# Kernel optimization log

Hardware: AMD Instinct MI355X
Metric: run time of the kernel (lower is better)

The kernel has to match this reference:

```python
import jax, jax.numpy as jnp
import numpy as np


def setup_inputs() -> dict:
    key = jax.random.key(0)
    ks = jax.random.split(key, 8)
    N, E = 100000, 3200000
    IN, H, OUT = 256, 128, 64
    x = jax.random.normal(ks[0], (N, IN), dtype=jnp.float32)
    src = jax.random.randint(ks[1], (E,), 0, N, dtype=jnp.int64)
    dst = jax.random.randint(ks[2], (E,), 0, N, dtype=jnp.int64)
    # Glorot-ish scaled weights
    W1_self = jax.random.normal(ks[3], (IN, H), dtype=jnp.float32) / np.sqrt(IN)
    W1_neigh = jax.random.normal(ks[4], (IN, H), dtype=jnp.float32) / np.sqrt(IN)
    b1 = jnp.zeros((H,), dtype=jnp.float32)
    W2_self = jax.random.normal(ks[5], (H, OUT), dtype=jnp.float32) / np.sqrt(H)
    W2_neigh = jax.random.normal(ks[6], (H, OUT), dtype=jnp.float32) / np.sqrt(H)
    b2 = jnp.zeros((OUT,), dtype=jnp.float32)
    return {"x": x, "src": src, "dst": dst,
            "W1_self": W1_self, "W1_neigh": W1_neigh, "b1": b1,
            "W2_self": W2_self, "W2_neigh": W2_neigh, "b2": b2}


def _sage_mean(h, src, dst, W_self, W_neigh, b, deg_inv):
    # mean aggregation over in-neighbors (edges src -> dst)
    N = h.shape[0]
    agg = jax.ops.segment_sum(h[src], dst, num_segments=N)  # [N, F]
    h_neigh = agg * deg_inv[:, None]
    return h @ W_self + h_neigh @ W_neigh + b


def reference(x, src, dst, W1_self, W1_neigh, b1, W2_self, W2_neigh, b2):
    N = x.shape[0]
    deg = jax.ops.segment_sum(jnp.ones_like(dst, dtype=x.dtype), dst, num_segments=N)
    deg_inv = 1.0 / jnp.maximum(deg, 1.0)  # DGL clamps in-degree to >= 1
    h = _sage_mean(x, src, dst, W1_self, W1_neigh, b1, deg_inv)
    h = jax.nn.relu(h)
    h = _sage_mean(h, src, dst, W2_self, W2_neigh, b2, deg_inv)
    return h
```

## Files before the change

### kernel.cpp

```cpp
#include <hip/hip_runtime.h>
#include <hip/hip_bf16.h>


typedef unsigned int uint32;
typedef __attribute__((ext_vector_type(8))) short short8;
typedef __attribute__((ext_vector_type(4))) float f32x4;

#define NBMAX 1024
#define EPB   8192

#if defined(__has_builtin)
#if __has_builtin(__builtin_amdgcn_cvt_pk_f32_fp8) && __has_builtin(__builtin_amdgcn_cvt_pk_fp8_f32)
#define FP8_HW 1
#endif
#endif
#ifndef FP8_HW
#define FP8_HW 0
#endif

__device__ __forceinline__ unsigned short f2bf(float f) {
    unsigned u = __float_as_uint(f);
    u += 0x7fffu + ((u >> 16) & 1u);
    return (unsigned short)(u >> 16);
}
__device__ __forceinline__ uint32 pack2bf(float lo, float hi) {
    return (uint32)f2bf(lo) | ((uint32)f2bf(hi) << 16);
}
__device__ __forceinline__ float bf_lo(uint32 v) { return __uint_as_float(v << 16); }
__device__ __forceinline__ float bf_hi(uint32 v) { return __uint_as_float(v & 0xFFFF0000u); }

__device__ __forceinline__ unsigned char enc8(float v) {
#if FP8_HW
    return (unsigned char)(__builtin_amdgcn_cvt_pk_fp8_f32(v, v, 0, false) & 0xFF);
#else
    float g = v * 0x1p-120f;
    uint32 b = __float_as_uint(g);
    uint32 s = (b >> 24) & 0x80u;
    b &= 0x7fffffffu;
    b += 0x7ffffu + ((b >> 20) & 1u);
    int t = (int)(b >> 20) - 960;
    t = t < 0 ? 0 : (t > 126 ? 126 : t);
    return (unsigned char)(s | (uint32)t);
#endif
}
#if !FP8_HW
__device__ __forceinline__ float dec1(uint32 b) {
    uint32 bits = ((b & 0x80u) << 24) | ((b & 0x7fu) << 20);
    return __uint_as_float(bits) * 0x1p+120f;
}
#endif
__device__ __forceinline__ void dec_u32(uint32 u, float& f0, float& f1, float& f2, float& f3) {
#if FP8_HW
    auto lo = __builtin_amdgcn_cvt_pk_f32_fp8(u, false);
    auto hi = __builtin_amdgcn_cvt_pk_f32_fp8(u, true);
    f0 = lo[0]; f1 = lo[1]; f2 = hi[0]; f3 = hi[1];
#else
    f0 = dec1(u & 0xffu); f1 = dec1((u >> 8) & 0xffu);
    f2 = dec1((u >> 16) & 0xffu); f3 = dec1(u >> 24);
#endif
}

__global__ __launch_bounds__(256) void k_bucket_count(const int* __restrict__ dst, int E,
                                                      int* __restrict__ bcnt) {
    __shared__ int hist[NBMAX];
    for (int i = threadIdx.x; i < NBMAX; i += 256) hist[i] = 0;
    __syncthreads();
    int base = blockIdx.x * EPB;
    #pragma unroll 4
    for (int i = 0; i < EPB / 256; ++i) {
        int e = base + i * 256 + threadIdx.x;
        if (e < E) atomicAdd(&hist[dst[e] >> 7], 1);
    }
    __syncthreads();
    for (int i = threadIdx.x; i < NBMAX; i += 256) {
        int h = hist[i];
        if (h) atomicAdd(&bcnt[i], h);
    }
}

__global__ __launch_bounds__(1024) void k_bucket_scan(const int* __restrict__ bcnt, int NB,
                                                      int* __restrict__ boffs, int* __restrict__ gfill,
                                                      int E) {
    __shared__ int sd[1024];
    int tid = threadIdx.x;
    int v = (tid < NB) ? bcnt[tid] : 0;
    sd[tid] = v;
    __syncthreads();
    for (int off = 1; off < 1024; off <<= 1) {
        int t = (tid >= off) ? sd[tid - off] : 0;
        __syncthreads();
        sd[tid] += t;
        __syncthreads();
    }
    int excl = sd[tid] - v;
    if (tid < NB) { boffs[tid] = excl; gfill[tid] = excl; }
    if (tid == 0) boffs[NB] = E;
}

__global__ __launch_bounds__(256) void k_bucket_scatter(const int* __restrict__ src,
                                                        const int* __restrict__ dst, int E,
                                                        int* __restrict__ gfill,
                                                        uint32* __restrict__ pairs) {
    __shared__ int hist[NBMAX];
    __shared__ int basea[NBMAX];
    for (int i = threadIdx.x; i < NBMAX; i += 256) hist[i] = 0;
    __syncthreads();
    int base = blockIdx.x * EPB;
    #pragma unroll 4
    for (int i = 0; i < EPB / 256; ++i) {
        int e = base + i * 256 + threadIdx.x;
        if (e < E) atomicAdd(&hist[dst[e] >> 7], 1);
    }
    __syncthreads();
    for (int i = threadIdx.x; i < NBMAX; i += 256) {
        int h = hist[i];
        basea[i] = h ? atomicAdd(&gfill[i], h) : 0;
        hist[i] = 0;
    }
    __syncthreads();
    #pragma unroll 4
    for (int i = 0; i < EPB / 256; ++i) {
        int e = base + i * 256 + threadIdx.x;
        if (e < E) {
            int d = dst[e];
            int b = d >> 7;
            int pos = basea[b] + atomicAdd(&hist[b], 1);
            pairs[pos] = ((uint32)src[e] << 7) | (uint32)(d & 127);
        }
    }
}

__global__ __launch_bounds__(256) void k_bucket_sort(const uint32* __restrict__ pairs,
                                                     const int* __restrict__ boffs,
                                                     int N, int E,
                                                     int* __restrict__ row_start,
                                                     float* __restrict__ deg_inv,
                                                     int* __restrict__ src_sorted) {
    __shared__ int cnt[128];
    __shared__ int sc[128];
    __shared__ int fill[128];
    int b = blockIdx.x, tid = threadIdx.x;
    int s0 = boffs[b], s1 = boffs[b + 1];
    if (tid < 128) cnt[tid] = 0;
    __syncthreads();
    for (int e = s0 + tid; e < s1; e += 256)
        atomicAdd(&cnt[pairs[e] & 127], 1);
    __syncthreads();
    if (tid < 128) sc[tid] = cnt[tid];
    __syncthreads();
    for (int off = 1; off < 128; off <<= 1) {
        int v = 0;
        if (tid < 128 && tid >= off) v = sc[tid - off];
        __syncthreads();
        if (tid < 128) sc[tid] += v;
        __syncthreads();
    }
    if (tid < 128) {
        int excl = sc[tid] - cnt[tid];
        int node = b * 128 + tid;
        if (node < N) {
            row_start[node] = s0 + excl;
            int d = cnt[tid];
            deg_inv[node] = 1.0f / (float)(d > 1 ? d : 1);
        }
        fill[tid] = s0 + excl;
    }
    if (b == 0 && tid == 0) row_start[N] = E;
    __syncthreads();
    for (int e = s0 + tid; e < s1; e += 256) {
        uint32 p = pairs[e];
        int pos = atomicAdd(&fill[p & 127], 1);
        src_sorted[pos] = (int)(p >> 7);
    }
}

__global__ __launch_bounds__(256) void k_wt(const float* __restrict__ Ws, const float* __restrict__ Wn,
                                            int K, int logK, int halfC, unsigned short* __restrict__ Wt) {
    int t = blockIdx.x * blockDim.x + threadIdx.x;
    int total = 2 * halfC * K;
    if (t >= total) return;
    int c = t >> logK, k = t & (K - 1);
    float v = (c < halfC) ? Ws[(size_t)k * halfC + c] : Wn[(size_t)k * halfC + (c - halfC)];
    Wt[t] = f2bf(v);
}

template<int K, bool AF32, bool YSPLIT>
__global__ __launch_bounds__(256) void gemm_rs(const void* __restrict__ Aptr, int Arows, int nstrip,
                                               const unsigned short* __restrict__ Wt,
                                               unsigned short* __restrict__ S16,
                                               unsigned char* __restrict__ N8) {
    constexpr int KS = K / 32;
    __shared__ unsigned short Bs[128 * K];
    const int tid = threadIdx.x;
    const int wave = tid >> 6, lane = tid & 63;
    const int l15 = lane & 15, l4 = lane >> 4;

    const unsigned short* Wtblk = Wt + (YSPLIT ? (size_t)blockIdx.y * 128 * K : 0);
    const bool out8_all = YSPLIT && (blockIdx.y == 1);

    for (int i = tid; i < 16 * K; i += 256) {
        int col = i / (K / 8);
        int cb  = (i % (K / 8)) * 16;
        int sb  = cb ^ ((col & 7) << 4);
        uint4 v = *reinterpret_cast<const uint4*>(&Wtblk[(size_t)col * K + (cb >> 1)]);
        *reinterpret_cast<uint4*>(&Bs[col * K + (sb >> 1)]) = v;
    }
    __syncthreads();

    const int stride = gridDim.x;
    int g = blockIdx.x;
    if (g >= nstrip) return;

    float4 aA[AF32 ? 2 * KS : 1], aB[AF32 ? 2 * KS : 1];
    uint4  uA[AF32 ? 1 : KS],     uB[AF32 ? 1 : KS];

    auto loadA = [&](int gg, float4* a, uint4* ub) {
        int arow = gg * 64 + wave * 16 + l15;
        if constexpr (AF32) {
            int r = arow < Arows ? arow : Arows - 1;
            const float* Ar = (const float*)Aptr + (size_t)r * K + l4 * 8;
            #pragma unroll
            for (int s = 0; s < KS; ++s) {
                a[2 * s]     = *reinterpret_cast<const float4*>(Ar + s * 32);
                a[2 * s + 1] = *reinterpret_cast<const float4*>(Ar + s * 32 + 4);
            }
        } else {
            const unsigned short* Ar = (const unsigned short*)Aptr + (size_t)arow * K + l4 * 8;
            #pragma unroll
            for (int s = 0; s < KS; ++s)
                ub[s] = *reinterpret_cast<const uint4*>(Ar + s * 32);
        }
    };

    auto compute = [&](int gc, float4* a, uint4* ub) {
        short8 af[KS];
        if constexpr (AF32) {
            #pragma unroll
            for (int s = 0; s < KS; ++s) {
                union { uint32 u[4]; short8 v; } cv;
                cv.u[0] = pack2bf(a[2*s].x,   a[2*s].y);
                cv.u[1] = pack2bf(a[2*s].z,   a[2*s].w);
                cv.u[2] = pack2bf(a[2*s+1].x, a[2*s+1].y);
                cv.u[3] = pack2bf(a[2*s+1].z, a[2*s+1].w);
                af[s] = cv.v;
            }
        } else {
            #pragma unroll
            for (int s = 0; s < KS; ++s) {
                union { uint4 q; short8 v; } cv;
                cv.q = ub[s];
                af[s] = cv.v;
            }
        }
        f32x4 acc[8] = {};
        #pragma unroll
        for (int s = 0; s < KS; ++s) {
            #pragma unroll
            for (int n = 0; n < 8; ++n) {
                int c = n * 16 + l15;
                int kb = s * 64 + l4 * 16;
                short8 bf = *reinterpret_cast<const short8*>(
                    &Bs[c * K + ((kb ^ ((c & 7) << 4)) >> 1)]);
                acc[n] = __builtin_amdgcn_mfma_f32_16x16x32_bf16(af[s], bf, acc[n], 0, 0, 0);
            }
        }
        const int rbase = gc * 64 + wave * 16;
        if constexpr (YSPLIT) {
            if (out8_all) {
                #pragma unroll
                for (int n = 0; n < 8; ++n) {
                    int col = n * 16 + l15;
                    #pragma unroll
                    for (int r = 0; r < 4; ++r) {
                        int rw = rbase + l4 * 4 + r;
                        N8[(size_t)rw * 128 + col] = enc8(acc[n][r]);
                    }
                }
            } else {
                #pragma unroll
                for (int n = 0; n < 8; ++n) {
                    int col = n * 16 + l15;
                    #pragma unroll
                    for (int r = 0; r < 4; ++r) {
                        int rw = rbase + l4 * 4 + r;
                        S16[(size_t)rw * 128 + col] = f2bf(acc[n][r]);
                    }
                }
            }
        } else {
            #pragma unroll
            for (int n = 0; n < 8; ++n) {
                #pragma unroll
                for (int r = 0; r < 4; ++r) {
                    int rw = rbase + l4 * 4 + r;
                    if (n < 4) S16[(size_t)rw * 64 + n * 16 + l15] = f2bf(acc[n][r]);
                    else       N8[(size_t)rw * 64 + (n - 4) * 16 + l15] = enc8(acc[n][r]);
                }
            }
        }
    };

    loadA(g, aA, uA);
    while (true) {
        int gn = g + stride;
        if (gn < nstrip) loadA(gn, aB, uB);
        compute(g, aA, uA);
        if (gn >= nstrip) break;
        g = gn;
        gn = g + stride;
        if (gn < nstrip) loadA(gn, aA, uA);
        compute(g, aB, uB);
        if (gn >= nstrip) break;
        g = gn;
    }
}

__global__ __launch_bounds__(256) void k_agg1(const uint2* __restrict__ t1n, const uint4* __restrict__ t1s,
                                              const int* __restrict__ rs, const int* __restrict__ ss,
                                              const float* __restrict__ dinv, const float* __restrict__ b1,
                                              uint4* __restrict__ h, int N) {
    int wid  = (blockIdx.x * blockDim.x + threadIdx.x) >> 6;
    int lane = threadIdx.x & 63;
    if (wid >= N) return;
    int e0 = rs[wid], e1 = rs[wid + 1];
    const int q = lane >> 4, c = lane & 15;
    float a0 = 0, a1 = 0, a2 = 0, a3 = 0, a4 = 0, a5 = 0, a6 = 0, a7 = 0;
    float f0, f1, f2, f3;
    int e = e0;
    for (; e + 16 <= e1; e += 16) {
        int s0 = ss[e + q];
        int s1 = ss[e + 4 + q];
        int s2 = ss[e + 8 + q];
        int s3 = ss[e + 12 + q];
        uint2 v0 = t1n[(size_t)s0 * 16 + c];
        uint2 v1 = t1n[(size_t)s1 * 16 + c];
        uint2 v2 = t1n[(size_t)s2 * 16 + c];
        uint2 v3 = t1n[(size_t)s3 * 16 + c];
        dec_u32(v0.x, f0, f1, f2, f3); a0 += f0; a1 += f1; a2 += f2; a3 += f3;
        dec_u32(v0.y, f0, f1, f2, f3); a4 += f0; a5 += f1; a6 += f2; a7 += f3;
        dec_u32(v1.x, f0, f1, f2, f3); a0 += f0; a1 += f1; a2 += f2; a3 += f3;
        dec_u32(v1.y, f0, f1, f2, f3); a4 += f0; a5 += f1; a6 += f2; a7 += f3;
        dec_u32(v2.x, f0, f1, f2, f3); a0 += f0; a1 += f1; a2 += f2; a3 += f3;
        dec_u32(v2.y, f0, f1, f2, f3); a4 += f0; a5 += f1; a6 += f2; a7 += f3;
        dec_u32(v3.x, f0, f1, f2, f3); a0 += f0; a1 += f1; a2 += f2; a3 += f3;
        dec_u32(v3.y, f0, f1, f2, f3); a4 += f0; a5 += f1; a6 += f2; a7 += f3;
    }
    for (; e < e1; e += 4) {
        if (e + q < e1) {
            int s = ss[e + q];
            uint2 v = t1n[(size_t)s * 16 + c];
            dec_u32(v.x, f0, f1, f2, f3); a0 += f0; a1 += f1; a2 += f2; a3 += f3;
            dec_u32(v.y, f0, f1, f2, f3); a4 += f0; a5 += f1; a6 += f2; a7 += f3;
        }
    }
    a0 += __shfl_xor(a0, 16); a1 += __shfl_xor(a1, 16); a2 += __shfl_xor(a2, 16); a3 += __shfl_xor(a3, 16);
    a4 += __shfl_xor(a4, 16); a5 += __shfl_xor(a5, 16); a6 += __shfl_xor(a6, 16); a7 += __shfl_xor(a7, 16);
    a0 += __shfl_xor(a0, 32); a1 += __shfl_xor(a1, 32); a2 += __shfl_xor(a2, 32); a3 += __shfl_xor(a3, 32);
    a4 += __shfl_xor(a4, 32); a5 += __shfl_xor(a5, 32); a6 += __shfl_xor(a6, 32); a7 += __shfl_xor(a7, 32);
    if (lane < 16) {
        float di = dinv[wid];
        uint4 sv = t1s[(size_t)wid * 16 + c];
        float4 bA = *reinterpret_cast<const float4*>(&b1[c * 8]);
        float4 bB = *reinterpret_cast<const float4*>(&b1[c * 8 + 4]);
        float h0 = fmaxf(fmaf(a0, di, bf_lo(sv.x)) + bA.x, 0.f);
        float h1 = fmaxf(fmaf(a1, di, bf_hi(sv.x)) + bA.y, 0.f);
        float h2 = fmaxf(fmaf(a2, di, bf_lo(sv.y)) + bA.z, 0.f);
        float h3 = fmaxf(fmaf(a3, di, bf_hi(sv.y)) + bA.w, 0.f);
        float h4 = fmaxf(fmaf(a4, di, bf_lo(sv.z)) + bB.x, 0.f);
        float h5 = fmaxf(fmaf(a5, di, bf_hi(sv.z)) + bB.y, 0.f);
        float h6 = fmaxf(fmaf(a6, di, bf_lo(sv.w)) + bB.z, 0.f);
        float h7 = fmaxf(fmaf(a7, di, bf_hi(sv.w)) + bB.w, 0.f);
        uint4 o;
        o.x = pack2bf(h0, h1); o.y = pack2bf(h2, h3);
        o.z = pack2bf(h4, h5); o.w = pack2bf(h6, h7);
        h[(size_t)wid * 16 + c] = o;
    }
}

__global__ __launch_bounds__(256) void k_agg2(const uint2* __restrict__ t2n, const uint4* __restrict__ t2s,
                                              const int* __restrict__ rs, const int* __restrict__ ss,
                                              const float* __restrict__ dinv, const float* __restrict__ b2,
                                              float* __restrict__ out, int N) {
    int wid  = (blockIdx.x * blockDim.x + threadIdx.x) >> 6;
    int lane = threadIdx.x & 63;
    if (wid >= N) return;
    int e0 = rs[wid], e1 = rs[wid + 1];
    const int o8 = lane >> 3, c = lane & 7;
    float a0 = 0, a1 = 0, a2 = 0, a3 = 0, a4 = 0, a5 = 0, a6 = 0, a7 = 0;
    float f0, f1, f2, f3;
    int e = e0;
    for (; e + 32 <= e1; e += 32) {
        int s0 = ss[e + o8];
        int s1 = ss[e + 8 + o8];
        int s2 = ss[e + 16 + o8];
        int s3 = ss[e + 24 + o8];
        uint2 v0 = t2n[(size_t)s0 * 8 + c];
        uint2 v1 = t2n[(size_t)s1 * 8 + c];
        uint2 v2 = t2n[(size_t)s2 * 8 + c];
        uint2 v3 = t2n[(size_t)s3 * 8 + c];
        dec_u32(v0.x, f0, f1, f2, f3); a0 += f0; a1 += f1; a2 += f2; a3 += f3;
        dec_u32(v0.y, f0, f1, f2, f3); a4 += f0; a5 += f1; a6 += f2; a7 += f3;
        dec_u32(v1.x, f0, f1, f2, f3); a0 += f0; a1 += f1; a2 += f2; a3 += f3;
        dec_u32(v1.y, f0, f1, f2, f3); a4 += f0; a5 += f1; a6 += f2; a7 += f3;
        dec_u32(v2.x, f0, f1, f2, f3); a0 += f0; a1 += f1; a2 += f2; a3 += f3;
        dec_u32(v2.y, f0, f1, f2, f3); a4 += f0; a5 += f1; a6 += f2; a7 += f3;
        dec_u32(v3.x, f0, f1, f2, f3); a0 += f0; a1 += f1; a2 += f2; a3 += f3;
        dec_u32(v3.y, f0, f1, f2, f3); a4 += f0; a5 += f1; a6 += f2; a7 += f3;
    }
    for (; e < e1; e += 8) {
        if (e + o8 < e1) {
            int s = ss[e + o8];
            uint2 v = t2n[(size_t)s * 8 + c];
            dec_u32(v.x, f0, f1, f2, f3); a0 += f0; a1 += f1; a2 += f2; a3 += f3;
            dec_u32(v.y, f0, f1, f2, f3); a4 += f0; a5 += f1; a6 += f2; a7 += f3;
        }
    }
    a0 += __shfl_xor(a0, 8);  a1 += __shfl_xor(a1, 8);  a2 += __shfl_xor(a2, 8);  a3 += __shfl_xor(a3, 8);
    a4 += __shfl_xor(a4, 8);  a5 += __shfl_xor(a5, 8);  a6 += __shfl_xor(a6, 8);  a7 += __shfl_xor(a7, 8);
    a0 += __shfl_xor(a0, 16); a1 += __shfl_xor(a1, 16); a2 += __shfl_xor(a2, 16); a3 += __shfl_xor(a3, 16);
    a4 += __shfl_xor(a4, 16); a5 += __shfl_xor(a5, 16); a6 += __shfl_xor(a6, 16); a7 += __shfl_xor(a7, 16);
    a0 += __shfl_xor(a0, 32); a1 += __shfl_xor(a1, 32); a2 += __shfl_xor(a2, 32); a3 += __shfl_xor(a3, 32);
    a4 += __shfl_xor(a4, 32); a5 += __shfl_xor(a5, 32); a6 += __shfl_xor(a6, 32); a7 += __shfl_xor(a7, 32);
    if (lane < 8) {
        float di = dinv[wid];
        uint4 sv = t2s[(size_t)wid * 8 + c];
        float4 bA = *reinterpret_cast<const float4*>(&b2[c * 8]);
        float4 bB = *reinterpret_cast<const float4*>(&b2[c * 8 + 4]);
        float4 oA, oB;
        oA.x = fmaf(a0, di, bf_lo(sv.x)) + bA.x;
        oA.y = fmaf(a1, di, bf_hi(sv.x)) + bA.y;
        oA.z = fmaf(a2, di, bf_lo(sv.y)) + bA.z;
        oA.w = fmaf(a3, di, bf_hi(sv.y)) + bA.w;
        oB.x = fmaf(a4, di, bf_lo(sv.z)) + bB.x;
        oB.y = fmaf(a5, di, bf_hi(sv.z)) + bB.y;
        oB.z = fmaf(a6, di, bf_lo(sv.w)) + bB.z;
        oB.w = fmaf(a7, di, bf_hi(sv.w)) + bB.w;
        *reinterpret_cast<float4*>(&out[(size_t)wid * 64 + c * 8]) = oA;
        *reinterpret_cast<float4*>(&out[(size_t)wid * 64 + c * 8 + 4]) = oB;
    }
}

extern "C" void kernel_launch(void* const* d_in, const int* in_sizes, int n_in,
                              void* d_out, int out_size, void* d_ws, size_t ws_size,
                              hipStream_t stream) {
    const float* x   = (const float*)d_in[0];
    const int*   src = (const int*)d_in[1];
    const int*   dst = (const int*)d_in[2];
    const float* W1s = (const float*)d_in[3];
    const float* W1n = (const float*)d_in[4];
    const float* b1  = (const float*)d_in[5];
    const float* W2s = (const float*)d_in[6];
    const float* W2n = (const float*)d_in[7];
    const float* b2  = (const float*)d_in[8];
    float* out = (float*)d_out;

    const int IN = 256, H = 128, OUT = 64;
    const int N  = in_sizes[0] / IN;
    const int E  = in_sizes[1];
    const int Mpad = (N + 127) & ~127;
    const int NB = (N + 127) >> 7;

    char* ws = (char*)d_ws;
    size_t off = 0;
    auto alloc = [&](size_t bytes) -> char* {
        char* p = ws + off;
        off = (off + bytes + 255) & ~(size_t)255;
        return p;
    };
    int*   row_start  = (int*)  alloc((size_t)(N + 1) * 4);
    float* deg_inv    = (float*)alloc((size_t)N * 4);
    int*   bcnt       = (int*)  alloc((size_t)NBMAX * 4);
    int*   boffs      = (int*)  alloc((size_t)(NBMAX + 1) * 4);
    int*   gfill      = (int*)  alloc((size_t)NBMAX * 4);
    int*   src_sorted = (int*)  alloc((size_t)E * 4);
    uint32* pairs     = (uint32*)alloc((size_t)E * 4);
    unsigned short* Wt1 = (unsigned short*)alloc((size_t)(2 * H) * IN * 2);
    unsigned short* Wt2 = (unsigned short*)alloc((size_t)(2 * OUT) * H * 2);
    unsigned short* t1s = (unsigned short*)alloc((size_t)Mpad * H * 2);
    unsigned char*  t1n = (unsigned char*) alloc((size_t)Mpad * H);
    unsigned short* hbf = (unsigned short*)alloc((size_t)Mpad * H * 2);

    hipMemsetAsync(bcnt, 0, (size_t)NBMAX * 4, stream);
    int nblk = (E + EPB - 1) / EPB;
    k_bucket_count  <<<nblk, 256, 0, stream>>>(dst, E, bcnt);
    k_bucket_scan   <<<1, 1024, 0, stream>>>(bcnt, NB, boffs, gfill, E);
    k_bucket_scatter<<<nblk, 256, 0, stream>>>(src, dst, E, gfill, pairs);
    k_bucket_sort   <<<NB, 256, 0, stream>>>(pairs, boffs, N, E, row_start, deg_inv, src_sorted);

    k_wt<<<(2 * H * IN + 255) / 256, 256, 0, stream>>>(W1s, W1n, IN, 8, H, Wt1);
    k_wt<<<(2 * OUT * H + 255) / 256, 256, 0, stream>>>(W2s, W2n, H, 7, OUT, Wt2);

    int nstrip1 = (N + 63) / 64;
    gemm_rs<256, true, true><<<dim3(512, 2), 256, 0, stream>>>(x, N, nstrip1, Wt1, t1s, t1n);
    k_agg1<<<(N + 3) / 4, 256, 0, stream>>>((const uint2*)t1n, (const uint4*)t1s,
                                            row_start, src_sorted, deg_inv, b1, (uint4*)hbf, N);
    int nstrip2 = Mpad / 64;
    gemm_rs<128, false, false><<<dim3(512, 1), 256, 0, stream>>>(hbf, Mpad, nstrip2, Wt2, t1s, t1n);
    k_agg2<<<(N + 3) / 4, 256, 0, stream>>>((const uint2*)t1n, (const uint4*)t1s,
                                            row_start, src_sorted, deg_inv, b2, out, N);
}
```

Baseline: 323.7 us.

## Split layer-1 GEMM into 64-column tiles with fragment-ordered LDS B layout

The layer-1 GEMM now runs over four 64-column y-slices instead of two 128-column ones, halving LDS for B and the per-thread accumulators so more blocks can be resident. B is stored in LDS in MFMA fragment order, so each lane reads one contiguous short8 per fragment with no XOR swizzle arithmetic. The double-buffered A register ping-pong becomes a single buffer, with the next strip's load issued after the current A is converted. In exchange, each x strip is read twice as often from global memory and there is less prefetch overlap.

```diff
diff --git a/kernel.cpp b/kernel.cpp
--- a/kernel.cpp
+++ b/kernel.cpp
@@ -184,37 +184,41 @@
     Wt[t] = f2bf(v);
 }
 
-template<int K, bool AF32, bool YSPLIT>
+template<int K, int NF, bool AF32, bool YSPLIT>
 __global__ __launch_bounds__(256) void gemm_rs(const void* __restrict__ Aptr, int Arows, int nstrip,
                                                const unsigned short* __restrict__ Wt,
                                                unsigned short* __restrict__ S16,
                                                unsigned char* __restrict__ N8) {
     constexpr int KS = K / 32;
-    __shared__ unsigned short Bs[128 * K];
+    __shared__ unsigned short Bs[NF * KS * 512];
     const int tid = threadIdx.x;
     const int wave = tid >> 6, lane = tid & 63;
     const int l15 = lane & 15, l4 = lane >> 4;
 
-    const unsigned short* Wtblk = Wt + (YSPLIT ? (size_t)blockIdx.y * 128 * K : 0);
-    const bool out8_all = YSPLIT && (blockIdx.y == 1);
-
-    for (int i = tid; i < 16 * K; i += 256) {
-        int col = i / (K / 8);
-        int cb  = (i % (K / 8)) * 16;
-        int sb  = cb ^ ((col & 7) << 4);
-        uint4 v = *reinterpret_cast<const uint4*>(&Wtblk[(size_t)col * K + (cb >> 1)]);
-        *reinterpret_cast<uint4*>(&Bs[col * K + (sb >> 1)]) = v;
-    }
-    __syncthreads();
-
+    const int ycol = YSPLIT ? blockIdx.y * 64 : 0;
+    const unsigned short* Wtblk = Wt + (size_t)ycol * K;
+    const bool out8 = YSPLIT && (blockIdx.y >= 2);
+    const int ybase = YSPLIT ? (blockIdx.y & 1) * 64 : 0;
+
+    for (int i = tid; i < NF * KS * 64; i += 256) {
+        int f = i >> 6, l = i & 63;
+        int s = f / NF, n = f - s * NF;
+        int col = n * 16 + (l & 15);
+        int k = s * 32 + (l >> 4) * 8;
+        uint4 v = *reinterpret_cast<const uint4*>(&Wtblk[(size_t)col * K + k]);
+        *reinterpret_cast<uint4*>(&Bs[(size_t)i * 8]) = v;
+    }
+    __syncthreads();
+
+    const unsigned short* Bl = Bs + (size_t)lane * 8;
     const int stride = gridDim.x;
     int g = blockIdx.x;
     if (g >= nstrip) return;
 
-    float4 aA[AF32 ? 2 * KS : 1], aB[AF32 ? 2 * KS : 1];
-    uint4  uA[AF32 ? 1 : KS],     uB[AF32 ? 1 : KS];
-
-    auto loadA = [&](int gg, float4* a, uint4* ub) {
+    float4 a[AF32 ? 2 * KS : 1];
+    uint4  ub[AF32 ? 1 : KS];
+
+    auto loadA = [&](int gg) {
         int arow = gg * 64 + wave * 16 + l15;
         if constexpr (AF32) {
             int r = arow < Arows ? arow : Arows - 1;
@@ -232,7 +236,8 @@
         }
     };
 
-    auto compute = [&](int gc, float4* a, uint4* ub) {
+    loadA(g);
+    while (true) {
         short8 af[KS];
         if constexpr (AF32) {
             #pragma unroll
@@ -252,64 +257,34 @@
                 af[s] = cv.v;
             }
         }
-        f32x4 acc[8] = {};
+        int gn = g + stride;
+        if (gn < nstrip) loadA(gn);
+
+        f32x4 acc[NF] = {};
         #pragma unroll
         for (int s = 0; s < KS; ++s) {
             #pragma unroll
-            for (int n = 0; n < 8; ++n) {
-                int c = n * 16 + l15;
-                int kb = s * 64 + l4 * 16;
-                short8 bf = *reinterpret_cast<const short8*>(
-                    &Bs[c * K + ((kb ^ ((c & 7) << 4)) >> 1)]);
+            for (int n = 0; n < NF; ++n) {
+                short8 bf = *reinterpret_cast<const short8*>(Bl + (size_t)(s * NF + n) * 512);
                 acc[n] = __builtin_amdgcn_mfma_f32_16x16x32_bf16(af[s], bf, acc[n], 0, 0, 0);
             }
         }
-        const int rbase = gc * 64 + wave * 16;
-        if constexpr (YSPLIT) {
-            if (out8_all) {
-                #pragma unroll
-                for (int n = 0; n < 8; ++n) {
-                    int col = n * 16 + l15;
-                    #pragma unroll
-                    for (int r = 0; r < 4; ++r) {
-                        int rw = rbase + l4 * 4 + r;
-                        N8[(size_t)rw * 128 + col] = enc8(acc[n][r]);
-                    }
-                }
-            } else {
-                #pragma unroll
-                for (int n = 0; n < 8; ++n) {
-                    int col = n * 16 + l15;
-                    #pragma unroll
-                    for (int r = 0; r < 4; ++r) {
-                        int rw = rbase + l4 * 4 + r;
-                        S16[(size_t)rw * 128 + col] = f2bf(acc[n][r]);
-                    }
-                }
-            }
-        } else {
-            #pragma unroll
-            for (int n = 0; n < 8; ++n) {
-                #pragma unroll
-                for (int r = 0; r < 4; ++r) {
-                    int rw = rbase + l4 * 4 + r;
+        const int rbase = g * 64 + wave * 16;
+        #pragma unroll
+        for (int n = 0; n < NF; ++n) {
+            #pragma unroll
+            for (int r = 0; r < 4; ++r) {
+                int rw = rbase + l4 * 4 + r;
+                if constexpr (YSPLIT) {
+                    int col = ybase + n * 16 + l15;
+                    if (out8) N8[(size_t)rw * 128 + col] = enc8(acc[n][r]);
+                    else      S16[(size_t)rw * 128 + col] = f2bf(acc[n][r]);
+                } else {
                     if (n < 4) S16[(size_t)rw * 64 + n * 16 + l15] = f2bf(acc[n][r]);
                     else       N8[(size_t)rw * 64 + (n - 4) * 16 + l15] = enc8(acc[n][r]);
                 }
             }
         }
-    };
-
-    loadA(g, aA, uA);
-    while (true) {
-        int gn = g + stride;
-        if (gn < nstrip) loadA(gn, aB, uB);
-        compute(g, aA, uA);
-        if (gn >= nstrip) break;
-        g = gn;
-        gn = g + stride;
-        if (gn < nstrip) loadA(gn, aA, uA);
-        compute(g, aB, uB);
         if (gn >= nstrip) break;
         g = gn;
     }
@@ -491,11 +466,11 @@
     k_wt<<<(2 * OUT * H + 255) / 256, 256, 0, stream>>>(W2s, W2n, H, 7, OUT, Wt2);
 
     int nstrip1 = (N + 63) / 64;
-    gemm_rs<256, true, true><<<dim3(512, 2), 256, 0, stream>>>(x, N, nstrip1, Wt1, t1s, t1n);
+    gemm_rs<256, 4, true, true><<<dim3(512, 4), 256, 0, stream>>>(x, N, nstrip1, Wt1, t1s, t1n);
     k_agg1<<<(N + 3) / 4, 256, 0, stream>>>((const uint2*)t1n, (const uint4*)t1s,
                                             row_start, src_sorted, deg_inv, b1, (uint4*)hbf, N);
     int nstrip2 = Mpad / 64;
-    gemm_rs<128, false, false><<<dim3(512, 1), 256, 0, stream>>>(hbf, Mpad, nstrip2, Wt2, t1s, t1n);
+    gemm_rs<128, 8, false, false><<<dim3(512, 1), 256, 0, stream>>>(hbf, Mpad, nstrip2, Wt2, t1s, t1n);
     k_agg2<<<(N + 3) / 4, 256, 0, stream>>>((const uint2*)t1n, (const uint4*)t1s,
                                             row_start, src_sorted, deg_inv, b2, out, N);
 }
```

Measured after the change: 348.7 us. 1.08x slower.
